# Kernel optimization log

Hardware: AMD Instinct MI355X
Metric: run time of the kernel (lower is better)

Reference implementation:

```python
import jax, jax.numpy as jnp
import numpy as np

MEM = 50   # memory_size
LA = 5     # look_ahead
EPS = 1e-5


def _tap_conv(h, taps, pad_left, pad_right):
    """Channel-independent temporal correlation with scalar taps.
    h: [B, L, H]; taps: [K]. out[t] = sum_j taps[j] * h[t + j - pad_left] (zero-padded).
    Returns [B, L + pad_left + pad_right - K + 1, H]."""
    B, L, H = h.shape
    K = taps.shape[0]
    xc = h.transpose(0, 2, 1).reshape(B * H, 1, L)
    k = taps.reshape(1, 1, K)
    out = jax.lax.conv_general_dilated(xc, k, (1,), [(pad_left, pad_right)],
                                       dimension_numbers=("NCH", "OIH", "NCH"))
    Lo = out.shape[-1]
    return out.reshape(B, H, Lo).transpose(0, 2, 1)


def _forward(x, W_lin, b_lin, mem_w, la_w, gamma, beta):
    B, L, D = x.shape
    H = W_lin.shape[0]
    # h = Linear(x); dropout is identity in eval mode
    h = jnp.einsum("bld,hd->blh", x, W_lin) + b_lin  # [B, L, H]

    # Source math: matmul(states^T, W[:k]).sum(-1) == sum_m states[:,m,:] * W[m,:].sum()
    wm = mem_w.sum(axis=-1)  # [MEM] scalar tap weights
    wf = la_w.sum(axis=-1)   # [LA]

    # --- memory (past) context ---
    # For t >= MEM: mem[t] = sum_j wm[j] * h[t - MEM + j]  (lag alignment)
    mem_conv = _tap_conv(h, wm, MEM, 0)[:, :L]  # [B, L, H]
    # For t < MEM: taps align to absolute times 0..t-1 with weights wm[0..t-1]
    wh = h[:, :MEM] * wm[None, :, None]                 # [B, MEM, H]
    pre = jnp.cumsum(wh, axis=1)                        # pre[t] = sum_{j<=t} wm[j] h[j]
    pref = jnp.concatenate([jnp.zeros((B, 1, H), h.dtype), pre[:, :MEM - 1]], axis=1)
    mem = jnp.concatenate([pref, mem_conv[:, MEM:]], axis=1)  # [B, L, H]

    # --- look-ahead (future) context ---
    # fut[t] = sum_j wf[j] * h[t + 1 + j], zero beyond L (truncation == zero pad)
    fut = _tap_conv(h, wf, 0, LA)[:, 1:L + 1]  # [B, L, H]

    out = h + mem + fut
    # LayerNorm over last dim
    mu = out.mean(axis=-1, keepdims=True)
    var = out.var(axis=-1, keepdims=True)
    out = (out - mu) * jax.lax.rsqrt(var + EPS) * gamma + beta
    return out


def setup_inputs() -> dict:
    key = jax.random.key(0)
    ks = jax.random.split(key, 5)
    B, L, D, H = 8, 2048, 1024, 2048
    x = jax.random.normal(ks[0], (B, L, D), jnp.float32)
    W_lin = jax.random.normal(ks[1], (H, D), jnp.float32) * (1.0 / np.sqrt(D))
    b_lin = jax.random.normal(ks[2], (H,), jnp.float32) * 0.01
    mem_w = jax.random.normal(ks[3], (MEM, H), jnp.float32)
    la_w = jax.random.normal(ks[4], (LA, H), jnp.float32)
    gamma = jnp.ones((H,), jnp.float32)
    beta = jnp.zeros((H,), jnp.float32)
    return {"x": x, "W_lin": W_lin, "b_lin": b_lin, "mem_w": mem_w,
            "la_w": la_w, "gamma": gamma, "beta": beta}


def reference(x, W_lin, b_lin, mem_w, la_w, gamma, beta):
    return _forward(x, W_lin, b_lin, mem_w, la_w, gamma, beta)
```

## Files before the change

kernel.cpp:

```cpp
#include <hip/hip_runtime.h>

typedef unsigned short u16;
typedef unsigned int u32;
typedef short bf16x8 __attribute__((ext_vector_type(8)));
typedef float f32x4 __attribute__((ext_vector_type(4)));

#define Ndim 2048
#define Kdim 1024
#define Lseq 2048
#define NT   16

__device__ __forceinline__ void gload_lds16(const void* g, void* l) {
    __builtin_amdgcn_global_load_lds(
        (const __attribute__((address_space(1))) u32*)(g),
        (__attribute__((address_space(3))) u32*)(l), 16, 0, 0);
}

__device__ __forceinline__ u16 f32_to_bf16(float f) {
    u32 u = __builtin_bit_cast(u32, f);
    u += 0x7FFFu + ((u >> 16) & 1u);
    return (u16)(u >> 16);
}

__device__ __forceinline__ u32 swz(u32 x) { return x ^ (((x >> 9) & 1u) << 5); }

__global__ __launch_bounds__(256) void cast_f32_bf16(
        const float* __restrict__ in, u16* __restrict__ out, int n8) {
    int i = blockIdx.x * 256 + threadIdx.x;
    if (i >= n8) return;
    const float4* p = (const float4*)(in + (size_t)i * 8);
    float4 a = p[0], b = p[1];
    float v[8] = {a.x, a.y, a.z, a.w, b.x, b.y, b.z, b.w};
    u32 o[4];
#pragma unroll
    for (int j = 0; j < 4; ++j) {
        u32 lo = f32_to_bf16(v[2 * j]);
        u32 hi = f32_to_bf16(v[2 * j + 1]);
        o[j] = lo | (hi << 16);
    }
    uint4 ov = make_uint4(o[0], o[1], o[2], o[3]);
    *(uint4*)(out + (size_t)i * 8) = ov;
}

__global__ __launch_bounds__(256) void taps_kernel(
        const float* __restrict__ mem_w, const float* __restrict__ la_w,
        float* __restrict__ cw) {
    int k = blockIdx.x;
    if (k == 50) {
        if (threadIdx.x == 0) cw[50] = 1.0f;
        return;
    }
    const float* src = (k < 50) ? (mem_w + (size_t)k * Ndim)
                                : (la_w + (size_t)(k - 51) * Ndim);
    float s = 0.f;
    for (int i = threadIdx.x; i < Ndim; i += 256) s += src[i];
#pragma unroll
    for (int off = 32; off; off >>= 1) s += __shfl_down(s, off);
    __shared__ float part[4];
    if ((threadIdx.x & 63) == 0) part[threadIdx.x >> 6] = s;
    __syncthreads();
    if (threadIdx.x == 0) cw[k] = part[0] + part[1] + part[2] + part[3];
}

__global__ __launch_bounds__(512, 1) void gemm8(
        const u16* __restrict__ A, const u16* __restrict__ Bw,
        const float* __restrict__ bias, u16* __restrict__ C) {
    __shared__ __align__(16) u16 smem[65536];
    char* sb = (char*)smem;

    const int tid = threadIdx.x;
    const int w = tid >> 6, lane = tid & 63;
    const int ln = lane & 15, kq = lane >> 4;
    const int wr = w >> 2, wc = w & 3;

    const int id0 = blockIdx.x;
    const int id = (id0 & 7) * 64 + (id0 >> 3);
    const int bm = id >> 3, bn = id & 7;

    const u32 aoff = (u32)(wr * 64 + ln) * 128 + (u32)kq * 16;
    const u32 boff = (u32)(wc * 32 + ln) * 128 + (u32)kq * 16;

    f32x4 acc[8][4] = {};

    auto stage = [&](int kt2, int which) {
        const int ah = which & 1;
        const bool isB = (which >> 1) != 0;
        const u16* src = isB ? Bw : A;
        const int rowbase = (isB ? bn * 256 : bm * 256) + ah * 128;
        const u32 dbase = (u32)(kt2 & 1) * 65536u + (isB ? 32768u : 0u) + (u32)ah * 16384u;
#pragma unroll
        for (int p = 0; p < 2; ++p) {
            u32 off = (u32)(p * 512 + tid) * 16;
            u32 soff = swz(off);
            u32 srow = soff >> 7, scol = (soff & 127u) >> 1;
            gload_lds16(src + (size_t)(rowbase + (int)srow) * Kdim + kt2 * 64 + (int)scol,
                        sb + dbase + off);
        }
    };

    stage(0, 0); stage(0, 1); stage(0, 2); stage(0, 3);
    stage(1, 0); stage(1, 2);
    asm volatile("s_waitcnt vmcnt(4)");
    __builtin_amdgcn_sched_barrier(0);
    __builtin_amdgcn_s_barrier();

    for (int kt = 0; kt < NT; ++kt) {
        const u32 bufb = (u32)(kt & 1) * 65536u;
#pragma unroll
        for (int q = 0; q < 4; ++q) {
            const int mh = q >> 1, nh = q & 1;
            bf16x8 a[4][2], b[2][2];
#pragma unroll
            for (int m = 0; m < 4; ++m)
#pragma unroll
                for (int ks = 0; ks < 2; ++ks)
                    a[m][ks] = *(const bf16x8*)(sb + bufb + (u32)mh * 16384u +
                                                swz(aoff + (u32)m * 2048u + (u32)ks * 64u));
#pragma unroll
            for (int n = 0; n < 2; ++n)
#pragma unroll
                for (int ks = 0; ks < 2; ++ks)
                    b[n][ks] = *(const bf16x8*)(sb + bufb + 32768u + (u32)nh * 16384u +
                                                swz(boff + (u32)n * 2048u + (u32)ks * 64u));
            if (q == 0)      { if (kt + 1 < NT) stage(kt + 1, 1); }
            else if (q == 1) { if (kt + 1 < NT) stage(kt + 1, 3); }
            else if (q == 2) { if (kt + 2 < NT) stage(kt + 2, 0); }
            else             { if (kt + 2 < NT) stage(kt + 2, 2); }
            __builtin_amdgcn_s_barrier();
            asm volatile("s_waitcnt lgkmcnt(0)");
            __builtin_amdgcn_sched_barrier(0);
            __builtin_amdgcn_s_setprio(1);
#pragma unroll
            for (int m = 0; m < 4; ++m)
#pragma unroll
                for (int n = 0; n < 2; ++n) {
                    acc[mh * 4 + m][nh * 2 + n] = __builtin_amdgcn_mfma_f32_16x16x32_bf16(
                        a[m][0], b[n][0], acc[mh * 4 + m][nh * 2 + n], 0, 0, 0);
                    acc[mh * 4 + m][nh * 2 + n] = __builtin_amdgcn_mfma_f32_16x16x32_bf16(
                        a[m][1], b[n][1], acc[mh * 4 + m][nh * 2 + n], 0, 0, 0);
                }
            __builtin_amdgcn_s_setprio(0);
            if (q == 3) {
                asm volatile("s_waitcnt vmcnt(4)");
                __builtin_amdgcn_sched_barrier(0);
            }
            __builtin_amdgcn_s_barrier();
        }
    }

    const int colbase = bn * 256 + wc * 32;
    const int rowbase = bm * 256 + wr * 64;
#pragma unroll
    for (int nh = 0; nh < 2; ++nh)
#pragma unroll
        for (int n = 0; n < 2; ++n) {
            int col = colbase + nh * 128 + n * 16 + ln;
            float bv = bias[col];
#pragma unroll
            for (int mh = 0; mh < 2; ++mh)
#pragma unroll
                for (int m = 0; m < 4; ++m) {
                    int row0 = rowbase + mh * 128 + m * 16 + kq * 4;
                    f32x4 v = acc[mh * 4 + m][nh * 2 + n];
#pragma unroll
                    for (int r = 0; r < 4; ++r)
                        C[(size_t)(row0 + r) * Ndim + col] = f32_to_bf16(v[r] + bv);
                }
        }
}

__global__ __launch_bounds__(256) void conv_ln(
        const u16* __restrict__ h, const float* __restrict__ cwg,
        const float* __restrict__ gamma, const float* __restrict__ beta,
        float* __restrict__ out) {
    const int tid = threadIdx.x;
    const int tb = blockIdx.x * 8;
    const int b = blockIdx.y;

    __shared__ float scw[70];
    __shared__ float red[4][8][2];
    if (tid < 70) scw[tid] = (tid >= 7 && tid < 63) ? cwg[tid - 7] : 0.f;
    __syncthreads();

    const u16* hb = h + (size_t)b * Lseq * Ndim;
    const int ch = tid * 8;
    float acc[8][8] = {};

    if (tb >= 50) {
        const int lrend = min(62, (Lseq - 1) - (tb - 50));
        const u16* rp = hb + (size_t)(tb - 50) * Ndim + ch;
        for (int lr = 0; lr <= lrend; ++lr) {
            uint4 u = *(const uint4*)rp;
            rp += Ndim;
            float hv[8];
            hv[0] = __builtin_bit_cast(float, u.x << 16);
            hv[1] = __builtin_bit_cast(float, u.x & 0xFFFF0000u);
            hv[2] = __builtin_bit_cast(float, u.y << 16);
            hv[3] = __builtin_bit_cast(float, u.y & 0xFFFF0000u);
            hv[4] = __builtin_bit_cast(float, u.z << 16);
            hv[5] = __builtin_bit_cast(float, u.z & 0xFFFF0000u);
            hv[6] = __builtin_bit_cast(float, u.w << 16);
            hv[7] = __builtin_bit_cast(float, u.w & 0xFFFF0000u);
#pragma unroll
            for (int t2 = 0; t2 < 8; ++t2) {
                float wgt = scw[lr - t2 + 7];
#pragma unroll
                for (int j = 0; j < 8; ++j)
                    acc[t2][j] = fmaf(wgt, hv[j], acc[t2][j]);
            }
        }
    } else {
        const int rmax = tb + 12;
        const u16* rp = hb + ch;
        for (int r = 0; r <= rmax; ++r) {
            uint4 u = *(const uint4*)rp;
            rp += Ndim;
            float hv[8];
            hv[0] = __builtin_bit_cast(float, u.x << 16);
            hv[1] = __builtin_bit_cast(float, u.x & 0xFFFF0000u);
            hv[2] = __builtin_bit_cast(float, u.y << 16);
            hv[3] = __builtin_bit_cast(float, u.y & 0xFFFF0000u);
            hv[4] = __builtin_bit_cast(float, u.z << 16);
            hv[5] = __builtin_bit_cast(float, u.z & 0xFFFF0000u);
            hv[6] = __builtin_bit_cast(float, u.w << 16);
            hv[7] = __builtin_bit_cast(float, u.w & 0xFFFF0000u);
#pragma unroll
            for (int t2 = 0; t2 < 8; ++t2) {
                int t = tb + t2;
                float wgt;
                if (t >= 50) {
                    int wi = r - t + 50;
                    wgt = ((unsigned)wi <= 55u) ? scw[wi + 7] : 0.f;
                } else if (r < t) {
                    wgt = scw[r + 7];
                } else {
                    int d = r - t;
                    wgt = (d <= 5) ? scw[50 + d + 7] : 0.f;
                }
#pragma unroll
                for (int j = 0; j < 8; ++j)
                    acc[t2][j] = fmaf(wgt, hv[j], acc[t2][j]);
            }
        }
    }

    float g[8], be[8];
    *(float4*)&g[0] = *(const float4*)(gamma + ch);
    *(float4*)&g[4] = *(const float4*)(gamma + ch + 4);
    *(float4*)&be[0] = *(const float4*)(beta + ch);
    *(float4*)&be[4] = *(const float4*)(beta + ch + 4);

    float s1v[8], s2v[8];
#pragma unroll
    for (int t2 = 0; t2 < 8; ++t2) {
        float s1 = 0.f, s2 = 0.f;
#pragma unroll
        for (int j = 0; j < 8; ++j) {
            s1 += acc[t2][j];
            s2 += acc[t2][j] * acc[t2][j];
        }
        s1v[t2] = s1;
        s2v[t2] = s2;
    }
#pragma unroll
    for (int off = 32; off; off >>= 1) {
#pragma unroll
        for (int t2 = 0; t2 < 8; ++t2) {
            s1v[t2] += __shfl_down(s1v[t2], off);
            s2v[t2] += __shfl_down(s2v[t2], off);
        }
    }
    const int wv = tid >> 6, lane = tid & 63;
    if (lane == 0) {
#pragma unroll
        for (int t2 = 0; t2 < 8; ++t2) {
            red[wv][t2][0] = s1v[t2];
            red[wv][t2][1] = s2v[t2];
        }
    }
    __syncthreads();
    const float inv = 1.0f / (float)Ndim;
#pragma unroll
    for (int t2 = 0; t2 < 8; ++t2) {
        float S1 = red[0][t2][0] + red[1][t2][0] + red[2][t2][0] + red[3][t2][0];
        float S2 = red[0][t2][1] + red[1][t2][1] + red[2][t2][1] + red[3][t2][1];
        float mu = S1 * inv;
        float var = S2 * inv - mu * mu;
        float rs = rsqrtf(var + 1e-5f);
        size_t base = ((size_t)(b * Lseq + tb + t2)) * Ndim + ch;
        float4 o0, o1;
        o0.x = (acc[t2][0] - mu) * rs * g[0] + be[0];
        o0.y = (acc[t2][1] - mu) * rs * g[1] + be[1];
        o0.z = (acc[t2][2] - mu) * rs * g[2] + be[2];
        o0.w = (acc[t2][3] - mu) * rs * g[3] + be[3];
        o1.x = (acc[t2][4] - mu) * rs * g[4] + be[4];
        o1.y = (acc[t2][5] - mu) * rs * g[5] + be[5];
        o1.z = (acc[t2][6] - mu) * rs * g[6] + be[6];
        o1.w = (acc[t2][7] - mu) * rs * g[7] + be[7];
        *(float4*)(out + base) = o0;
        *(float4*)(out + base + 4) = o1;
    }
}

extern "C" void kernel_launch(void* const* d_in, const int* in_sizes, int n_in,
                              void* d_out, int out_size, void* d_ws, size_t ws_size,
                              hipStream_t stream) {
    const float* x     = (const float*)d_in[0];
    const float* W     = (const float*)d_in[1];
    const float* b_lin = (const float*)d_in[2];
    const float* mem_w = (const float*)d_in[3];
    const float* la_w  = (const float*)d_in[4];
    const float* gamma = (const float*)d_in[5];
    const float* beta  = (const float*)d_in[6];
    float* out = (float*)d_out;

    u16* xb = (u16*)d_ws;
    u16* wb = xb + (size_t)16777216;
    u16* hb = wb + (size_t)2097152;
    float* cw = (float*)(hb + (size_t)33554432);

    taps_kernel<<<dim3(56), dim3(256), 0, stream>>>(mem_w, la_w, cw);
    cast_f32_bf16<<<dim3(8192), dim3(256), 0, stream>>>(x, xb, 2097152);
    cast_f32_bf16<<<dim3(1024), dim3(256), 0, stream>>>(W, wb, 262144);
    gemm8<<<dim3(512), dim3(512), 0, stream>>>(xb, wb, b_lin, hb);
    conv_ln<<<dim3(256, 8), dim3(256), 0, stream>>>(hb, cw, gamma, beta, out);
}
```

Measured before the change: 376.8 us.

## Split GEMM LDS tiles by K-half with new swizzle; widen conv_ln time tile

The GEMM's LDS layout now stores each 64-wide K slice as two 32-wide halves with 64-byte rows and an extra XOR bit in the swizzle. This is meant to reduce LDS bank conflicts on the MFMA operand reads. The conv_ln kernel now uses 512 threads, each covering 4 channels and 16 timesteps, with blocks remapped across batches. Each h row load is therefore reused over more output times, cutting redundant halo reads, at the cost of more accumulator registers per thread.

```diff
diff --git a/kernel.cpp b/kernel.cpp
--- a/kernel.cpp
+++ b/kernel.cpp
@@ -22,7 +22,9 @@
     return (u16)(u >> 16);
 }
 
-__device__ __forceinline__ u32 swz(u32 x) { return x ^ (((x >> 9) & 1u) << 5); }
+__device__ __forceinline__ u32 swz(u32 x) {
+    return x ^ (((x >> 9) & 1u) << 5) ^ (((x >> 8) & 1u) << 4);
+}
 
 __global__ __launch_bounds__(256) void cast_f32_bf16(
         const float* __restrict__ in, u16* __restrict__ out, int n8) {
@@ -77,8 +79,8 @@
     const int id = (id0 & 7) * 64 + (id0 >> 3);
     const int bm = id >> 3, bn = id & 7;
 
-    const u32 aoff = (u32)(wr * 64 + ln) * 128 + (u32)kq * 16;
-    const u32 boff = (u32)(wc * 32 + ln) * 128 + (u32)kq * 16;
+    const u32 aoff = (u32)(wr * 64 + ln) * 64 + (u32)kq * 16;
+    const u32 boff = (u32)(wc * 32 + ln) * 64 + (u32)kq * 16;
 
     f32x4 acc[8][4] = {};
 
@@ -92,8 +94,10 @@
         for (int p = 0; p < 2; ++p) {
             u32 off = (u32)(p * 512 + tid) * 16;
             u32 soff = swz(off);
-            u32 srow = soff >> 7, scol = (soff & 127u) >> 1;
-            gload_lds16(src + (size_t)(rowbase + (int)srow) * Kdim + kt2 * 64 + (int)scol,
+            u32 ks  = off >> 13;
+            u32 row = (off >> 6) & 127u;
+            u32 kc  = (soff & 63u) >> 1;
+            gload_lds16(src + (size_t)(rowbase + (int)row) * Kdim + kt2 * 64 + (int)(ks * 32u + kc),
                         sb + dbase + off);
         }
     };
@@ -115,13 +119,13 @@
 #pragma unroll
                 for (int ks = 0; ks < 2; ++ks)
                     a[m][ks] = *(const bf16x8*)(sb + bufb + (u32)mh * 16384u +
-                                                swz(aoff + (u32)m * 2048u + (u32)ks * 64u));
+                                                swz(aoff + (u32)m * 1024u + (u32)ks * 8192u));
 #pragma unroll
             for (int n = 0; n < 2; ++n)
 #pragma unroll
                 for (int ks = 0; ks < 2; ++ks)
                     b[n][ks] = *(const bf16x8*)(sb + bufb + 32768u + (u32)nh * 16384u +
-                                                swz(boff + (u32)n * 2048u + (u32)ks * 64u));
+                                                swz(boff + (u32)n * 1024u + (u32)ks * 8192u));
             if (q == 0)      { if (kt + 1 < NT) stage(kt + 1, 1); }
             else if (q == 1) { if (kt + 1 < NT) stage(kt + 1, 3); }
             else if (q == 2) { if (kt + 2 < NT) stage(kt + 2, 0); }
@@ -169,93 +173,85 @@
         }
 }
 
-__global__ __launch_bounds__(256) void conv_ln(
+__global__ __launch_bounds__(512) void conv_ln(
         const u16* __restrict__ h, const float* __restrict__ cwg,
         const float* __restrict__ gamma, const float* __restrict__ beta,
         float* __restrict__ out) {
     const int tid = threadIdx.x;
-    const int tb = blockIdx.x * 8;
-    const int b = blockIdx.y;
-
-    __shared__ float scw[70];
-    __shared__ float red[4][8][2];
-    if (tid < 70) scw[tid] = (tid >= 7 && tid < 63) ? cwg[tid - 7] : 0.f;
+    const int id0 = (blockIdx.y << 7) + blockIdx.x;
+    const int id = (id0 & 7) * 128 + (id0 >> 3);
+    const int b = id >> 7;
+    const int tb = (id & 127) * 16;
+
+    __shared__ float scw[86];
+    __shared__ float red[8][16][2];
+    if (tid < 86) scw[tid] = (tid >= 15 && tid < 71) ? cwg[tid - 15] : 0.f;
     __syncthreads();
 
     const u16* hb = h + (size_t)b * Lseq * Ndim;
-    const int ch = tid * 8;
-    float acc[8][8] = {};
+    const int ch = tid * 4;
+    float acc[16][4] = {};
 
     if (tb >= 50) {
-        const int lrend = min(62, (Lseq - 1) - (tb - 50));
+        const int lrend = min(70, (Lseq - 1) - (tb - 50));
         const u16* rp = hb + (size_t)(tb - 50) * Ndim + ch;
         for (int lr = 0; lr <= lrend; ++lr) {
-            uint4 u = *(const uint4*)rp;
+            uint2 u = *(const uint2*)rp;
             rp += Ndim;
-            float hv[8];
+            float hv[4];
             hv[0] = __builtin_bit_cast(float, u.x << 16);
             hv[1] = __builtin_bit_cast(float, u.x & 0xFFFF0000u);
             hv[2] = __builtin_bit_cast(float, u.y << 16);
             hv[3] = __builtin_bit_cast(float, u.y & 0xFFFF0000u);
-            hv[4] = __builtin_bit_cast(float, u.z << 16);
-            hv[5] = __builtin_bit_cast(float, u.z & 0xFFFF0000u);
-            hv[6] = __builtin_bit_cast(float, u.w << 16);
-            hv[7] = __builtin_bit_cast(float, u.w & 0xFFFF0000u);
-#pragma unroll
-            for (int t2 = 0; t2 < 8; ++t2) {
-                float wgt = scw[lr - t2 + 7];
-#pragma unroll
-                for (int j = 0; j < 8; ++j)
+#pragma unroll
+            for (int t2 = 0; t2 < 16; ++t2) {
+                float wgt = scw[lr - t2 + 15];
+#pragma unroll
+                for (int j = 0; j < 4; ++j)
                     acc[t2][j] = fmaf(wgt, hv[j], acc[t2][j]);
             }
         }
     } else {
-        const int rmax = tb + 12;
+        const int rmax = tb + 20;
         const u16* rp = hb + ch;
         for (int r = 0; r <= rmax; ++r) {
-            uint4 u = *(const uint4*)rp;
+            uint2 u = *(const uint2*)rp;
             rp += Ndim;
-            float hv[8];
+            float hv[4];
             hv[0] = __builtin_bit_cast(float, u.x << 16);
             hv[1] = __builtin_bit_cast(float, u.x & 0xFFFF0000u);
             hv[2] = __builtin_bit_cast(float, u.y << 16);
             hv[3] = __builtin_bit_cast(float, u.y & 0xFFFF0000u);
-            hv[4] = __builtin_bit_cast(float, u.z << 16);
-            hv[5] = __builtin_bit_cast(float, u.z & 0xFFFF0000u);
-            hv[6] = __builtin_bit_cast(float, u.w << 16);
-            hv[7] = __builtin_bit_cast(float, u.w & 0xFFFF0000u);
-#pragma unroll
-            for (int t2 = 0; t2 < 8; ++t2) {
+#pragma unroll
+            for (int t2 = 0; t2 < 16; ++t2) {
                 int t = tb + t2;
                 float wgt;
                 if (t >= 50) {
                     int wi = r - t + 50;
-                    wgt = ((unsigned)wi <= 55u) ? scw[wi + 7] : 0.f;
+                    wgt = ((unsigned)wi <= 55u) ? scw[wi + 15] : 0.f;
                 } else if (r < t) {
-                    wgt = scw[r + 7];
+                    wgt = scw[r + 15];
                 } else {
                     int d = r - t;
-                    wgt = (d <= 5) ? scw[50 + d + 7] : 0.f;
+                    wgt = (d <= 5) ? scw[50 + d + 15] : 0.f;
                 }
 #pragma unroll
-                for (int j = 0; j < 8; ++j)
+                for (int j = 0; j < 4; ++j)
                     acc[t2][j] = fmaf(wgt, hv[j], acc[t2][j]);
             }
         }
     }
 
-    float g[8], be[8];
+    float g[4], be[4];
     *(float4*)&g[0] = *(const float4*)(gamma + ch);
-    *(float4*)&g[4] = *(const float4*)(gamma + ch + 4);
     *(float4*)&be[0] = *(const float4*)(beta + ch);
-    *(float4*)&be[4] = *(const float4*)(beta + ch + 4);
-
-    float s1v[8], s2v[8];
-#pragma unroll
-    for (int t2 = 0; t2 < 8; ++t2) {
+
+    float s1v[16], s2v[16];
+#pragma unroll
+    for (int t2 = 0; t2 < 16; ++t2) {
         float s1 = 0.f, s2 = 0.f;
 #pragma unroll
-        for (int j = 0; j < 8; ++j) {
+        for (int j = 0; j < 4; ++j) {
             s1 += acc[t2][j];
             s2 += acc[t2][j] * acc[t2][j];
         }
@@ -265,7 +261,7 @@
 #pragma unroll
     for (int off = 32; off; off >>= 1) {
 #pragma unroll
-        for (int t2 = 0; t2 < 8; ++t2) {
+        for (int t2 = 0; t2 < 16; ++t2) {
             s1v[t2] += __shfl_down(s1v[t2], off);
             s2v[t2] += __shfl_down(s2v[t2], off);
         }
@@ -273,7 +269,7 @@
     const int wv = tid >> 6, lane = tid & 63;
     if (lane == 0) {
 #pragma unroll
-        for (int t2 = 0; t2 < 8; ++t2) {
+        for (int t2 = 0; t2 < 16; ++t2) {
             red[wv][t2][0] = s1v[t2];
             red[wv][t2][1] = s2v[t2];
         }
@@ -281,24 +277,23 @@
     __syncthreads();
     const float inv = 1.0f / (float)Ndim;
 #pragma unroll
-    for (int t2 = 0; t2 < 8; ++t2) {
-        float S1 = red[0][t2][0] + red[1][t2][0] + red[2][t2][0] + red[3][t2][0];
-        float S2 = red[0][t2][1] + red[1][t2][1] + red[2][t2][1] + red[3][t2][1];
+    for (int t2 = 0; t2 < 16; ++t2) {
+        float S1 = 0.f, S2 = 0.f;
+#pragma unroll
+        for (int wv2 = 0; wv2 < 8; ++wv2) {
+            S1 += red[wv2][t2][0];
+            S2 += red[wv2][t2][1];
+        }
         float mu = S1 * inv;
         float var = S2 * inv - mu * mu;
         float rs = rsqrtf(var + 1e-5f);
         size_t base = ((size_t)(b * Lseq + tb + t2)) * Ndim + ch;
-        float4 o0, o1;
-        o0.x = (acc[t2][0] - mu) * rs * g[0] + be[0];
-        o0.y = (acc[t2][1] - mu) * rs * g[1] + be[1];
-        o0.z = (acc[t2][2] - mu) * rs * g[2] + be[2];
-        o0.w = (acc[t2][3] - mu) * rs * g[3] + be[3];
-        o1.x = (acc[t2][4] - mu) * rs * g[4] + be[4];
-        o1.y = (acc[t2][5] - mu) * rs * g[5] + be[5];
-        o1.z = (acc[t2][6] - mu) * rs * g[6] + be[6];
-        o1.w = (acc[t2][7] - mu) * rs * g[7] + be[7];
-        *(float4*)(out + base) = o0;
-        *(float4*)(out + base + 4) = o1;
+        float4 o;
+        o.x = (acc[t2][0] - mu) * rs * g[0] + be[0];
+        o.y = (acc[t2][1] - mu) * rs * g[1] + be[1];
+        o.z = (acc[t2][2] - mu) * rs * g[2] + be[2];
+        o.w = (acc[t2][3] - mu) * rs * g[3] + be[3];
+        *(float4*)(out + base) = o;
     }
 }
 
@@ -323,5 +318,5 @@
     cast_f32_bf16<<<dim3(8192), dim3(256), 0, stream>>>(x, xb, 2097152);
     cast_f32_bf16<<<dim3(1024), dim3(256), 0, stream>>>(W, wb, 262144);
     gemm8<<<dim3(512), dim3(512), 0, stream>>>(xb, wb, b_lin, hb);
-    conv_ln<<<dim3(256, 8), dim3(256), 0, stream>>>(hb, cw, gamma, beta, out);
-}
+    conv_ln<<<dim3(128, 8), dim3(512), 0, stream>>>(hb, cw, gamma, beta, out);
+}
```

New measurement: 405.1 us. 7.5% more time.
